# Kernel optimization log

Measured on AMD Instinct MI355X. Metric: run time of the kernel, lower is better.

The kernel has to match this reference:

```python
import jax, jax.numpy as jnp
import numpy as np

GROUPS = 32
EPS = 1e-6


def group_norm(x, gamma, beta):
    b, c, h, w = x.shape
    xg = x.reshape(b, GROUPS, c // GROUPS, h, w)
    mu = xg.mean(axis=(2, 3, 4), keepdims=True)
    var = xg.var(axis=(2, 3, 4), keepdims=True)
    xn = ((xg - mu) * jax.lax.rsqrt(var + EPS)).reshape(b, c, h, w)
    return xn * gamma[None, :, None, None] + beta[None, :, None, None]


def conv1x1(x, w, b):
    # x: (b,c_in,h,w), w: (c_out,c_in), b: (c_out,)
    return jnp.einsum('oc,bchw->bohw', w, x) + b[None, :, None, None]


def setup_inputs() -> dict:
    key = jax.random.key(0)
    ks = jax.random.split(key, 10)
    c = 512
    scale = 1.0 / np.sqrt(c)
    inp = jax.random.normal(ks[0], (16, c, 32, 32), dtype=jnp.float32)
    return {
        'inp': inp,
        'gamma': jnp.ones((c,), jnp.float32),
        'beta': jnp.zeros((c,), jnp.float32),
        'Wq': jax.random.normal(ks[1], (c, c), jnp.float32) * scale,
        'bq': jnp.zeros((c,), jnp.float32),
        'Wk': jax.random.normal(ks[2], (c, c), jnp.float32) * scale,
        'bk': jnp.zeros((c,), jnp.float32),
        'Wv': jax.random.normal(ks[3], (c, c), jnp.float32) * scale,
        'bv': jnp.zeros((c,), jnp.float32),
        'Wo': jax.random.normal(ks[4], (c, c), jnp.float32) * scale,
        'bo': jnp.zeros((c,), jnp.float32),
    }


def reference(inp, gamma, beta, Wq, bq, Wk, bk, Wv, bv, Wo, bo):
    b, c, h, w = inp.shape
    x = group_norm(inp, gamma, beta)
    Q = conv1x1(x, Wq, bq).reshape(b, c, h * w)  # (b,c,n)
    K = conv1x1(x, Wk, bk).reshape(b, c, h * w)  # (b,c,m)
    V = conv1x1(x, Wv, bv).reshape(b, c, h * w)  # (b,c,m)
    # attn[b,n,m] = sum_c Q[b,c,n] * K[b,c,m], scaled then softmax over m
    attn = jnp.einsum('bcn,bcm->bnm', Q, K) / jnp.sqrt(jnp.float32(c))
    attn = jax.nn.softmax(attn, axis=2)
    # A[b,c,n] = sum_m V[b,c,m] * attn[b,n,m]  (== bmm(V, attn^T))
    A = jnp.einsum('bcm,bnm->bcn', V, attn).reshape(b, c, h, w)
    A = conv1x1(A, Wo, bo)
    return inp + A
```

## Files before the change

kernel.cpp:

```cpp
#include <hip/hip_runtime.h>

typedef unsigned short UST;
typedef __attribute__((ext_vector_type(8))) short bf16x8;
typedef __attribute__((ext_vector_type(8))) unsigned short us8;
typedef __attribute__((ext_vector_type(4))) float f32x4;

__device__ __forceinline__ UST f2bf(float f) {
  union { float f; unsigned int u; } x; x.f = f;
  unsigned int r = x.u + 0x7fffu + ((x.u >> 16) & 1u);
  return (UST)(r >> 16);
}
__device__ __forceinline__ float bf2f(UST h) {
  union { unsigned int u; float f; } x; x.u = ((unsigned int)h) << 16;
  return x.f;
}

typedef const __attribute__((address_space(1))) unsigned int* gptr32;
typedef __attribute__((address_space(3))) unsigned int* lptr32;

__device__ __forceinline__ void load16(const void* g, void* l) {
  __builtin_amdgcn_global_load_lds((gptr32)(unsigned long long)g,
                                   (lptr32)(unsigned int)(unsigned long long)l,
                                   16, 0, 0);
}

__global__ __launch_bounds__(256) void conv_w(
    const float4* __restrict__ a, const float4* __restrict__ b,
    const float4* __restrict__ c, const float4* __restrict__ d,
    ushort4* __restrict__ oa, ushort4* __restrict__ ob,
    ushort4* __restrict__ oc, ushort4* __restrict__ od,
    const float4* __restrict__ bq4, const float4* __restrict__ bk4,
    float4* __restrict__ bqk4) {
  int i = blockIdx.x * 256 + threadIdx.x;
  float4 v;
  v = a[i]; oa[i] = make_ushort4(f2bf(v.x), f2bf(v.y), f2bf(v.z), f2bf(v.w));
  v = b[i]; ob[i] = make_ushort4(f2bf(v.x), f2bf(v.y), f2bf(v.z), f2bf(v.w));
  v = c[i]; oc[i] = make_ushort4(f2bf(v.x), f2bf(v.y), f2bf(v.z), f2bf(v.w));
  v = d[i]; od[i] = make_ushort4(f2bf(v.x), f2bf(v.y), f2bf(v.z), f2bf(v.w));
  if (blockIdx.x == 0) {
    int t = threadIdx.x;
    bqk4[t] = (t < 128) ? bq4[t] : bk4[t - 128];
  }
}

__global__ __launch_bounds__(256) void gn_fused(
    const float* __restrict__ inp, const float* __restrict__ gamma,
    const float* __restrict__ beta, UST* __restrict__ Xnt) {
  const int g = blockIdx.x & 31, b = blockIdx.x >> 5;
  const int tid = threadIdx.x;
  const float* base = inp + ((size_t)b * 32 + g) * 16384;
  const float4* p4 = (const float4*)base;
  float s = 0.f, ss = 0.f;
#pragma unroll
  for (int i = 0; i < 16; i++) {
    float4 t = p4[tid + i * 256];
    s += t.x + t.y + t.z + t.w;
    ss += t.x * t.x + t.y * t.y + t.z * t.z + t.w * t.w;
  }
  for (int o = 32; o >= 1; o >>= 1) { s += __shfl_xor(s, o); ss += __shfl_xor(ss, o); }
  __shared__ float red[8];
  __shared__ float mu_s, rstd_s;
  const int w = tid >> 6;
  if ((tid & 63) == 0) { red[w * 2] = s; red[w * 2 + 1] = ss; }
  __syncthreads();
  if (tid == 0) {
    float S1 = red[0] + red[2] + red[4] + red[6];
    float S2 = red[1] + red[3] + red[5] + red[7];
    float mu = S1 * (1.f / 16384.f);
    float var = S2 * (1.f / 16384.f) - mu * mu;
    mu_s = mu; rstd_s = rsqrtf(var + 1e-6f);
  }
  __syncthreads();
  const float mu = mu_s, rstd = rstd_s;
#pragma unroll
  for (int cc = 0; cc < 2; cc++) {
    const int ccg = g * 2 + cc;
    float sc[8], sh[8];
#pragma unroll
    for (int j = 0; j < 8; j++) {
      int ch = ccg * 8 + j;
      sc[j] = gamma[ch] * rstd;
      sh[j] = beta[ch] - mu * sc[j];
    }
#pragma unroll
    for (int i = 0; i < 4; i++) {
      const int n = tid + i * 256;
      us8 v;
#pragma unroll
      for (int j = 0; j < 8; j++) {
        float x = inp[((size_t)b * 512 + ccg * 8 + j) * 1024 + n];
        v[j] = f2bf(x * sc[j] + sh[j]);
      }
      *(us8*)(Xnt + (size_t)b * 524288 + (size_t)ccg * 8192 + (size_t)n * 8) = v;
    }
  }
}

__global__ __launch_bounds__(256) void softmax_k(const UST* __restrict__ S,
                                                 UST* __restrict__ P) {
  const int w = threadIdx.x >> 6, lane = threadIdx.x & 63;
  const size_t row = (size_t)blockIdx.x * 4 + w;
  const us8* Sr = (const us8*)(S + row * 1024);
  us8 a = Sr[lane], b = Sr[64 + lane];
  float v[16];
#pragma unroll
  for (int j = 0; j < 8; j++) { v[j] = bf2f(a[j]); v[8 + j] = bf2f(b[j]); }
  float m = v[0];
#pragma unroll
  for (int i = 1; i < 16; i++) m = fmaxf(m, v[i]);
#pragma unroll
  for (int o = 32; o >= 1; o >>= 1) m = fmaxf(m, __shfl_xor(m, o));
  float s = 0.f;
#pragma unroll
  for (int i = 0; i < 16; i++) { v[i] = __expf(v[i] - m); s += v[i]; }
#pragma unroll
  for (int o = 32; o >= 1; o >>= 1) s += __shfl_xor(s, o);
  const float rs = 1.f / s;
  us8* Pr = (us8*)(P + row * 1024);
  us8 oa, ob;
#pragma unroll
  for (int j = 0; j < 8; j++) { oa[j] = f2bf(v[j] * rs); ob[j] = f2bf(v[8 + j] * rs); }
  Pr[lane] = oa; Pr[64 + lane] = ob;
}

template <int EPI>
__global__ __launch_bounds__(256, 2) void gemm_bt(
    const UST* __restrict__ A, const UST* __restrict__ B, void* __restrict__ C,
    const float* __restrict__ bias, const float* __restrict__ extra, float scale,
    int N, int K, int ldc,
    int rsA, int csA, int ssA, int rsB, int csB, int ssB,
    long zA, long zB, long zC) {
  __shared__ __align__(16) UST lA[128 * 32];
  __shared__ __align__(16) UST lB[128 * 32];

  const int tid = threadIdx.x;
  const int z = blockIdx.z;
  const int m0 = blockIdx.y * 128;
  const int n0 = blockIdx.x * 128;
  const UST* Ab = A + (long)z * zA;
  const UST* Bb = B + (long)z * zB;

  const int w = tid >> 6, lane = tid & 63;
  const int quad = lane >> 4, l16 = lane & 15;
  const int wm = w >> 1, wn = w & 1;

  f32x4 acc[4][4];
#pragma unroll
  for (int i = 0; i < 4; i++)
#pragma unroll
    for (int j = 0; j < 4; j++) acc[i][j] = f32x4{0.f, 0.f, 0.f, 0.f};

  const int rowa = tid >> 2;
  const int kchunk = tid & 3;
  const UST* gA = Ab + (size_t)(m0 + rowa) * rsA + (size_t)kchunk * csA;
  const UST* gB = Bb + (size_t)(n0 + rowa) * rsB + (size_t)kchunk * csB;
  char* lAw = (char*)lA + (w << 10);
  char* lBw = (char*)lB + (w << 10);

  for (int k0 = 0; k0 < K; k0 += 32) {
    __syncthreads();
    load16(gA, lAw);
    load16(gA + (size_t)64 * rsA, lAw + 4096);
    load16(gB, lBw);
    load16(gB + (size_t)64 * rsB, lBw + 4096);
    gA += ssA; gB += ssB;
    __syncthreads();
    bf16x8 af[4], bfr[4];
#pragma unroll
    for (int i = 0; i < 4; i++)
      af[i] = *(const bf16x8*)(lA + (wm * 64 + i * 16 + l16) * 32 + quad * 8);
#pragma unroll
    for (int j = 0; j < 4; j++)
      bfr[j] = *(const bf16x8*)(lB + (wn * 64 + j * 16 + l16) * 32 + quad * 8);
#pragma unroll
    for (int i = 0; i < 4; i++)
#pragma unroll
      for (int j = 0; j < 4; j++)
        acc[i][j] = __builtin_amdgcn_mfma_f32_16x16x32_bf16(af[i], bfr[j], acc[i][j], 0, 0, 0);
  }

  const int gr0 = m0 + wm * 64 + quad * 4;
  const int gc0 = n0 + wn * 64 + l16;
  if constexpr (EPI == 4) {
    float* Cb = (float*)C + (long)z * zC;
#pragma unroll
    for (int i = 0; i < 4; i++)
#pragma unroll
      for (int j = 0; j < 4; j++) {
        const int gc = gc0 + j * 16;
#pragma unroll
        for (int r = 0; r < 4; r++) {
          const int gr = gr0 + i * 16 + r;
          float v = acc[i][j][r] + bias[gr] + extra[(long)z * zC + (size_t)gr * ldc + gc];
          Cb[(size_t)gr * ldc + gc] = v;
        }
      }
  } else {
    UST* Cb = (UST*)C + (long)z * zC;
#pragma unroll
    for (int i = 0; i < 4; i++)
#pragma unroll
      for (int j = 0; j < 4; j++) {
        const int gc = gc0 + j * 16;
        float bc = 0.f;
        if constexpr (EPI == 0) bc = bias[gc];
#pragma unroll
        for (int r = 0; r < 4; r++) {
          const int gr = gr0 + i * 16 + r;
          float v = acc[i][j][r] + bc;
          if constexpr (EPI == 1) v += bias[gr];
          if constexpr (EPI == 5) v *= scale;
          Cb[(size_t)gr * ldc + gc] = f2bf(v);
        }
      }
  }
}

extern "C" void kernel_launch(void* const* d_in, const int* in_sizes, int n_in,
                              void* d_out, int out_size, void* d_ws, size_t ws_size,
                              hipStream_t stream) {
  const float* inp   = (const float*)d_in[0];
  const float* gamma = (const float*)d_in[1];
  const float* beta  = (const float*)d_in[2];
  const float* Wq    = (const float*)d_in[3];
  const float* bq    = (const float*)d_in[4];
  const float* Wk    = (const float*)d_in[5];
  const float* bk    = (const float*)d_in[6];
  const float* Wv    = (const float*)d_in[7];
  const float* bv    = (const float*)d_in[8];
  const float* Wo    = (const float*)d_in[9];
  const float* bo    = (const float*)d_in[10];
  float* out = (float*)d_out;
  char* ws = (char*)d_ws;

  UST*   Xnt  = (UST*)(ws);
  UST*   QKt  = (UST*)(ws + ((size_t)16 << 20));
  UST*   V    = (UST*)(ws + ((size_t)48 << 20));
  UST*   S    = (UST*)(ws + ((size_t)64 << 20));
  float* bqk  = (float*)(ws + ((size_t)96 << 20));
  UST*   Wqkb = (UST*)(ws + ((size_t)96 << 20) + 8192);
  UST*   Wvb  = Wqkb + 524288;
  UST*   Wob  = Wvb + 262144;
  UST*   P    = QKt;
  UST*   At   = Xnt;

  conv_w<<<256, 256, 0, stream>>>(
      (const float4*)Wq, (const float4*)Wk, (const float4*)Wv, (const float4*)Wo,
      (ushort4*)Wqkb, (ushort4*)(Wqkb + 262144), (ushort4*)Wvb, (ushort4*)Wob,
      (const float4*)bq, (const float4*)bk, (float4*)bqk);
  gn_fused<<<512, 256, 0, stream>>>(inp, gamma, beta, Xnt);

  gemm_bt<0><<<dim3(8, 8, 16), 256, 0, stream>>>(
      Xnt, Wqkb, QKt, bqk, nullptr, 1.f,
      1024, 512, 1024, 8, 8192, 32768, 512, 8, 32, 524288, 0, 1048576);
  gemm_bt<1><<<dim3(8, 4, 16), 256, 0, stream>>>(
      Wvb, Xnt, V, bv, nullptr, 1.f,
      1024, 512, 1024, 512, 8, 32, 8, 8192, 32768, 0, 524288, 524288);
  gemm_bt<5><<<dim3(8, 8, 16), 256, 0, stream>>>(
      QKt, QKt + 512, S, nullptr, nullptr, 0.04419417382415922f,
      1024, 512, 1024, 1024, 8, 32, 1024, 8, 32, 1048576, 1048576, 1048576);
  softmax_k<<<4096, 256, 0, stream>>>(S, P);
  gemm_bt<3><<<dim3(4, 8, 16), 256, 0, stream>>>(
      P, V, At, nullptr, nullptr, 1.f,
      512, 1024, 512, 1024, 8, 32, 1024, 8, 32, 1048576, 524288, 524288);
  gemm_bt<4><<<dim3(8, 4, 16), 256, 0, stream>>>(
      Wob, At, out, bo, inp, 1.f,
      1024, 512, 1024, 512, 8, 32, 512, 8, 32, 0, 524288, 524288);
}
```

Measured before the change: 245.1 us.

## Fuse Q/K/V projections into one GEMM and stage epilogues through LDS

Concatenates the Wq, Wk and Wv bf16 weights and their biases so that a single GEMM launch computes Q, K and V. The V tiles are written transposed through LDS into the separate V buffer. All GEMM epilogues now stage the accumulator tile in shared memory and write coalesced 16-byte vectors, and the final fp32 residual epilogue does the same with float4 loads and stores. This removes one kernel launch and the scattered 2-byte and 4-byte global stores. The cost is extra LDS traffic, extra barriers and a larger shared buffer, which may reduce occupancy.

```diff
diff --git a/kernel.cpp b/kernel.cpp
--- a/kernel.cpp
+++ b/kernel.cpp
@@ -25,21 +25,20 @@
 }
 
 __global__ __launch_bounds__(256) void conv_w(
-    const float4* __restrict__ a, const float4* __restrict__ b,
-    const float4* __restrict__ c, const float4* __restrict__ d,
-    ushort4* __restrict__ oa, ushort4* __restrict__ ob,
-    ushort4* __restrict__ oc, ushort4* __restrict__ od,
+    const float4* __restrict__ wq, const float4* __restrict__ wk,
+    const float4* __restrict__ wv, const float4* __restrict__ wo,
+    ushort4* __restrict__ oqkv, ushort4* __restrict__ owo,
     const float4* __restrict__ bq4, const float4* __restrict__ bk4,
-    float4* __restrict__ bqk4) {
+    const float4* __restrict__ bv4, float4* __restrict__ bqkv4) {
   int i = blockIdx.x * 256 + threadIdx.x;
   float4 v;
-  v = a[i]; oa[i] = make_ushort4(f2bf(v.x), f2bf(v.y), f2bf(v.z), f2bf(v.w));
-  v = b[i]; ob[i] = make_ushort4(f2bf(v.x), f2bf(v.y), f2bf(v.z), f2bf(v.w));
-  v = c[i]; oc[i] = make_ushort4(f2bf(v.x), f2bf(v.y), f2bf(v.z), f2bf(v.w));
-  v = d[i]; od[i] = make_ushort4(f2bf(v.x), f2bf(v.y), f2bf(v.z), f2bf(v.w));
-  if (blockIdx.x == 0) {
-    int t = threadIdx.x;
-    bqk4[t] = (t < 128) ? bq4[t] : bk4[t - 128];
+  v = wq[i]; oqkv[i]          = make_ushort4(f2bf(v.x), f2bf(v.y), f2bf(v.z), f2bf(v.w));
+  v = wk[i]; oqkv[i + 65536]  = make_ushort4(f2bf(v.x), f2bf(v.y), f2bf(v.z), f2bf(v.w));
+  v = wv[i]; oqkv[i + 131072] = make_ushort4(f2bf(v.x), f2bf(v.y), f2bf(v.z), f2bf(v.w));
+  v = wo[i]; owo[i]           = make_ushort4(f2bf(v.x), f2bf(v.y), f2bf(v.z), f2bf(v.w));
+  if (blockIdx.x < 2) {
+    int t = blockIdx.x * 256 + threadIdx.x;
+    if (t < 384) bqkv4[t] = (t < 128) ? bq4[t] : (t < 256 ? bk4[t - 128] : bv4[t - 256]);
   }
 }
 
@@ -127,11 +126,12 @@
 __global__ __launch_bounds__(256, 2) void gemm_bt(
     const UST* __restrict__ A, const UST* __restrict__ B, void* __restrict__ C,
     const float* __restrict__ bias, const float* __restrict__ extra, float scale,
-    int N, int K, int ldc,
+    int K, int ldc,
     int rsA, int csA, int ssA, int rsB, int csB, int ssB,
     long zA, long zB, long zC) {
-  __shared__ __align__(16) UST lA[128 * 32];
-  __shared__ __align__(16) UST lB[128 * 32];
+  __shared__ __align__(16) UST buf[17408];
+  UST* lA = buf;
+  UST* lB = buf + 4096;
 
   const int tid = threadIdx.x;
   const int z = blockIdx.z;
@@ -179,40 +179,76 @@
         acc[i][j] = __builtin_amdgcn_mfma_f32_16x16x32_bf16(af[i], bfr[j], acc[i][j], 0, 0, 0);
   }
 
-  const int gr0 = m0 + wm * 64 + quad * 4;
-  const int gc0 = n0 + wn * 64 + l16;
+  __syncthreads();
+
   if constexpr (EPI == 4) {
+    float* fbuf = (float*)buf;
     float* Cb = (float*)C + (long)z * zC;
+    const float* Eb = extra + (long)z * zC;
+#pragma unroll
+    for (int h = 0; h < 2; h++) {
+      if (wm == h) {
+#pragma unroll
+        for (int i = 0; i < 4; i++)
+#pragma unroll
+          for (int j = 0; j < 4; j++)
+#pragma unroll
+            for (int r = 0; r < 4; r++)
+              fbuf[(i * 16 + quad * 4 + r) * 132 + wn * 64 + j * 16 + l16] = acc[i][j][r];
+      }
+      __syncthreads();
+#pragma unroll
+      for (int it = 0; it < 8; it++) {
+        int q = tid + it * 256;
+        int row = q >> 5, colc = q & 31;
+        int gr = m0 + h * 64 + row;
+        size_t off = (size_t)gr * ldc + n0 + colc * 4;
+        float4 v = *(float4*)&fbuf[row * 132 + colc * 4];
+        float4 e = *(const float4*)&Eb[off];
+        float bb = bias[gr];
+        v.x += bb + e.x; v.y += bb + e.y; v.z += bb + e.z; v.w += bb + e.w;
+        *(float4*)&Cb[off] = v;
+      }
+      __syncthreads();
+    }
+  } else {
+    const bool vreg = (EPI == 6) && (n0 >= 1024);
 #pragma unroll
     for (int i = 0; i < 4; i++)
 #pragma unroll
       for (int j = 0; j < 4; j++) {
-        const int gc = gc0 + j * 16;
+        float bc = 0.f;
+        if constexpr (EPI == 6) bc = bias[n0 + wn * 64 + j * 16 + l16];
 #pragma unroll
         for (int r = 0; r < 4; r++) {
-          const int gr = gr0 + i * 16 + r;
-          float v = acc[i][j][r] + bias[gr] + extra[(long)z * zC + (size_t)gr * ldc + gc];
-          Cb[(size_t)gr * ldc + gc] = v;
+          float v = acc[i][j][r] + bc;
+          if constexpr (EPI == 5) v *= scale;
+          const int lr = wm * 64 + i * 16 + quad * 4 + r;
+          const int lc = wn * 64 + j * 16 + l16;
+          if (!vreg) buf[lr * 136 + lc] = f2bf(v);
+          else       buf[lc * 136 + lr] = f2bf(v);
         }
       }
-  } else {
-    UST* Cb = (UST*)C + (long)z * zC;
-#pragma unroll
-    for (int i = 0; i < 4; i++)
-#pragma unroll
-      for (int j = 0; j < 4; j++) {
-        const int gc = gc0 + j * 16;
-        float bc = 0.f;
-        if constexpr (EPI == 0) bc = bias[gc];
-#pragma unroll
-        for (int r = 0; r < 4; r++) {
-          const int gr = gr0 + i * 16 + r;
-          float v = acc[i][j][r] + bc;
-          if constexpr (EPI == 1) v += bias[gr];
-          if constexpr (EPI == 5) v *= scale;
-          Cb[(size_t)gr * ldc + gc] = f2bf(v);
-        }
-      }
+    __syncthreads();
+    if (!vreg) {
+      UST* Cb = (UST*)C + (long)z * zC;
+#pragma unroll
+      for (int it = 0; it < 8; it++) {
+        int q = tid + it * 256;
+        int row = q >> 4, colc = q & 15;
+        us8 v = *(us8*)&buf[row * 136 + colc * 8];
+        *(us8*)&Cb[(size_t)(m0 + row) * ldc + n0 + colc * 8] = v;
+      }
+    } else {
+      UST* Vb = (UST*)extra + (long)z * 524288;
+#pragma unroll
+      for (int it = 0; it < 8; it++) {
+        int q = tid + it * 256;
+        int c = q >> 4, mc = q & 15;
+        us8 v = *(us8*)&buf[c * 136 + mc * 8];
+        *(us8*)&Vb[(size_t)(n0 - 1024 + c) * 1024 + m0 + mc * 8] = v;
+      }
+    }
   }
 }
 
@@ -233,37 +269,33 @@
   float* out = (float*)d_out;
   char* ws = (char*)d_ws;
 
-  UST*   Xnt  = (UST*)(ws);
-  UST*   QKt  = (UST*)(ws + ((size_t)16 << 20));
-  UST*   V    = (UST*)(ws + ((size_t)48 << 20));
-  UST*   S    = (UST*)(ws + ((size_t)64 << 20));
-  float* bqk  = (float*)(ws + ((size_t)96 << 20));
-  UST*   Wqkb = (UST*)(ws + ((size_t)96 << 20) + 8192);
-  UST*   Wvb  = Wqkb + 524288;
-  UST*   Wob  = Wvb + 262144;
-  UST*   P    = QKt;
-  UST*   At   = Xnt;
+  UST*   Xnt   = (UST*)(ws);
+  UST*   QKt   = (UST*)(ws + ((size_t)16 << 20));
+  UST*   V     = (UST*)(ws + ((size_t)48 << 20));
+  UST*   S     = (UST*)(ws + ((size_t)64 << 20));
+  float* bqkv  = (float*)(ws + ((size_t)96 << 20));
+  UST*   Wqkvb = (UST*)(ws + ((size_t)96 << 20) + 8192);
+  UST*   Wob   = Wqkvb + 786432;
+  UST*   P     = QKt;
+  UST*   At    = Xnt;
 
   conv_w<<<256, 256, 0, stream>>>(
       (const float4*)Wq, (const float4*)Wk, (const float4*)Wv, (const float4*)Wo,
-      (ushort4*)Wqkb, (ushort4*)(Wqkb + 262144), (ushort4*)Wvb, (ushort4*)Wob,
-      (const float4*)bq, (const float4*)bk, (float4*)bqk);
+      (ushort4*)Wqkvb, (ushort4*)Wob,
+      (const float4*)bq, (const float4*)bk, (const float4*)bv, (float4*)bqkv);
   gn_fused<<<512, 256, 0, stream>>>(inp, gamma, beta, Xnt);
 
-  gemm_bt<0><<<dim3(8, 8, 16), 256, 0, stream>>>(
-      Xnt, Wqkb, QKt, bqk, nullptr, 1.f,
-      1024, 512, 1024, 8, 8192, 32768, 512, 8, 32, 524288, 0, 1048576);
-  gemm_bt<1><<<dim3(8, 4, 16), 256, 0, stream>>>(
-      Wvb, Xnt, V, bv, nullptr, 1.f,
-      1024, 512, 1024, 512, 8, 32, 8, 8192, 32768, 0, 524288, 524288);
+  gemm_bt<6><<<dim3(12, 8, 16), 256, 0, stream>>>(
+      Xnt, Wqkvb, QKt, bqkv, (const float*)V, 1.f,
+      512, 1024, 8, 8192, 32768, 512, 8, 32, 524288, 0, 1048576);
   gemm_bt<5><<<dim3(8, 8, 16), 256, 0, stream>>>(
       QKt, QKt + 512, S, nullptr, nullptr, 0.04419417382415922f,
-      1024, 512, 1024, 1024, 8, 32, 1024, 8, 32, 1048576, 1048576, 1048576);
+      512, 1024, 1024, 8, 32, 1024, 8, 32, 1048576, 1048576, 1048576);
   softmax_k<<<4096, 256, 0, stream>>>(S, P);
   gemm_bt<3><<<dim3(4, 8, 16), 256, 0, stream>>>(
       P, V, At, nullptr, nullptr, 1.f,
-      512, 1024, 512, 1024, 8, 32, 1024, 8, 32, 1048576, 524288, 524288);
+      1024, 512, 1024, 8, 32, 1024, 8, 32, 1048576, 524288, 524288);
   gemm_bt<4><<<dim3(8, 4, 16), 256, 0, stream>>>(
       Wob, At, out, bo, inp, 1.f,
-      1024, 512, 1024, 512, 8, 32, 512, 8, 32, 0, 524288, 524288);
-}
+      512, 1024, 512, 8, 32, 512, 8, 32, 0, 524288, 524288);
+}
```

After: 244.9 us. No clear change (-0.1%).
